# Kernel optimization log

Measured on AMD Instinct MI355X. Metric: run time of the kernel, lower is better.

## Reference

```python
import jax, jax.numpy as jnp
import numpy as np

N = 50000      # nodes
E = 800000     # edges (before self-loops)
IN = 256       # in_channels
H = 4          # heads (layer 1)
C = 64         # hidden per head
OUT = 40       # out_channels / classes


def setup_inputs() -> dict:
    key = jax.random.key(0)
    ks = jax.random.split(key, 10)
    s = 0.05  # weight init scale
    return {
        "x": jax.random.normal(ks[0], (N, IN), jnp.float32),
        "edge_index": jax.random.randint(ks[1], (2, E), 0, N),
        "W1": jax.random.normal(ks[2], (IN, H * C), jnp.float32) * s,
        "a_src1": jax.random.normal(ks[3], (H, C), jnp.float32) * s,
        "a_dst1": jax.random.normal(ks[4], (H, C), jnp.float32) * s,
        "b1": jnp.zeros((H * C,), jnp.float32),
        "W2": jax.random.normal(ks[5], (H * C, OUT), jnp.float32) * s,
        "a_src2": jax.random.normal(ks[6], (1, OUT), jnp.float32) * s,
        "a_dst2": jax.random.normal(ks[7], (1, OUT), jnp.float32) * s,
        "b2": jnp.zeros((OUT,), jnp.float32),
    }


def _gat_layer(x, src, dst, W, a_src, a_dst, bias, heads, out_c):
    """PyG GATConv (concat=True, negative_slope=0.2, self-loops already in src/dst)."""
    n = x.shape[0]
    h = (x @ W).reshape(n, heads, out_c)                    # [N,H,C]
    al_s = jnp.sum(h * a_src, axis=-1)                      # [N,H]
    al_d = jnp.sum(h * a_dst, axis=-1)                      # [N,H]
    e = jax.nn.leaky_relu(al_s[src] + al_d[dst], 0.2)       # [Etot,H]
    # edge softmax over incoming edges of each destination node
    m = jax.ops.segment_max(e, dst, num_segments=n)         # [N,H]
    ee = jnp.exp(e - m[dst])
    denom = jax.ops.segment_sum(ee, dst, num_segments=n)
    alpha = ee / (denom[dst] + 1e-16)                       # [Etot,H]
    msg = alpha[:, :, None] * h[src]                        # [Etot,H,C]
    out = jax.ops.segment_sum(msg, dst, num_segments=n)     # [N,H,C]
    return out.reshape(n, heads * out_c) + bias


def reference(x, edge_index, W1, a_src1, a_dst1, b1, W2, a_src2, a_dst2, b2):
    n = x.shape[0]
    loops = jnp.arange(n, dtype=edge_index.dtype)
    src = jnp.concatenate([edge_index[0], loops])
    dst = jnp.concatenate([edge_index[1], loops])
    h = _gat_layer(x, src, dst, W1, a_src1, a_dst1, b1, H, C)   # [N, H*C]
    h = jax.nn.relu(h)
    # F.dropout in eval mode is identity (reference run in eval mode)
    out = _gat_layer(h, src, dst, W2, a_src2, a_dst2, b2, 1, OUT)  # [N, OUT]
    return jax.nn.log_softmax(out, axis=1)
```

## Files before the change

kernel.cpp:

```cpp
#include <hip/hip_runtime.h>
#include <hip/hip_bf16.h>

typedef __hip_bfloat16 bf16;
typedef short v8s __attribute__((ext_vector_type(8)));
typedef float v4f __attribute__((ext_vector_type(4)));

constexpr int NN    = 50000;
constexpr int NE    = 800000;
constexpr int CIN   = 256;
constexpr int HC    = 256;
constexpr int NH    = 4;
constexpr int NOUT  = 40;
constexpr int NPAD  = 48;
constexpr int SCB   = 196;
constexpr int B1    = 128;
constexpr int CH    = (NE + B1 - 1) / B1;
constexpr int NB    = (NN + 255) >> 8;

constexpr size_t al256(size_t x){ return (x + 255) & ~(size_t)255; }
constexpr size_t WS_FLAGS = 0;
constexpr size_t WS_EW1   = 256;
constexpr size_t WS_W1T   = al256(WS_EW1   + (size_t)NE*16);
constexpr size_t WS_AS1N  = al256(WS_W1T   + (size_t)CIN*HC*2);
constexpr size_t WS_AD1N  = al256(WS_AS1N  + HC*2);
constexpr size_t WS_B1N   = al256(WS_AD1N  + HC*2);
constexpr size_t WS_W2T   = al256(WS_B1N   + HC*2);
constexpr size_t WS_AS2N  = al256(WS_W2T   + (size_t)NPAD*HC*2);
constexpr size_t WS_AD2N  = al256(WS_AS2N  + NOUT*2);
constexpr size_t WS_B2N   = al256(WS_AD2N  + NOUT*2);
constexpr size_t WS_COUNTS= al256(WS_B2N   + NOUT*2);
constexpr size_t WS_CURSOR= al256(WS_COUNTS+ (size_t)NN*4);
constexpr size_t WS_ROWPTR= al256(WS_CURSOR+ (size_t)NN*4);
constexpr size_t WS_EIDX  = al256(WS_ROWPTR+ (size_t)(NN+1)*4);
constexpr size_t WS_H1    = al256(WS_EIDX  + (size_t)NE*4);
constexpr size_t WS_ALS1  = al256(WS_H1    + (size_t)NN*HC);
constexpr size_t WS_ALD1  = al256(WS_ALS1  + (size_t)NN*NH*4);
constexpr size_t WS_Y1    = al256(WS_ALD1  + (size_t)NN*NH*4);
constexpr size_t WS_H2    = al256(WS_Y1    + (size_t)NN*HC*2);
constexpr size_t WS_ALS2  = al256(WS_H2    + (size_t)NN*64);
constexpr size_t WS_ALD2  = al256(WS_ALS2  + (size_t)NN*4);
constexpr size_t WS_EW2   = al256(WS_ALD2  + (size_t)NN*4);
constexpr size_t WS_BSUM  = al256(WS_EW2   + (size_t)NE*4);
constexpr size_t WS_BOFF  = al256(WS_BSUM  + 1024);
constexpr size_t WS_GCNT  = al256(WS_BOFF  + 1024);
constexpr size_t WS_ROFF  = al256(WS_GCNT  + (size_t)256*B1*4);
constexpr size_t WS_BBASE = al256(WS_ROFF  + (size_t)256*B1*4);
constexpr size_t WS_EBUF  = al256(WS_BBASE + 1056);

constexpr int CV_W1  = 0;
constexpr int CV_AS1 = CV_W1  + CIN*HC;
constexpr int CV_AD1 = CV_AS1 + HC;
constexpr int CV_B1  = CV_AD1 + HC;
constexpr int CV_W2  = CV_B1  + HC;
constexpr int CV_AS2 = CV_W2  + HC*NOUT;
constexpr int CV_AD2 = CV_AS2 + NOUT;
constexpr int CV_B2  = CV_AD2 + NOUT;
constexpr int CV_HIST= CV_B2  + NOUT;
constexpr int CV_END = CV_HIST + NE;

__device__ __forceinline__ float b2f(bf16 v) { return __bfloat162float(v); }
__device__ __forceinline__ bf16  f2b(float v){ return __float2bfloat16(v); }
__device__ __forceinline__ float bits2f(unsigned short u){ return __uint_as_float(((unsigned)u) << 16); }
__device__ __forceinline__ unsigned short f2bits(float v){
  bf16 t = __float2bfloat16(v);
  return *reinterpret_cast<unsigned short*>(&t);
}
__device__ __forceinline__ float lrelu(float x){ return x > 0.f ? x : 0.2f * x; }

__device__ __forceinline__ float wave_sum(float v){
  #pragma unroll
  for (int off = 32; off; off >>= 1) v += __shfl_xor(v, off, 64);
  return v;
}
__device__ __forceinline__ float wave_max(float v){
  #pragma unroll
  for (int off = 32; off; off >>= 1) v = fmaxf(v, __shfl_xor(v, off, 64));
  return v;
}

__global__ __launch_bounds__(64) void k_detect(const unsigned short* __restrict__ xu,
                                               const unsigned* __restrict__ eu,
                                               int* __restrict__ flags){
  int lane = threadIdx.x;
  int cnt = 0;
  for (int i = lane; i < 256; i += 64){
    int e = (xu[i] >> 7) & 0xFF;
    cnt += (e >= 0x60 && e <= 0x8F) ? 1 : 0;
  }
  #pragma unroll
  for (int off = 32; off; off >>= 1) cnt += __shfl_xor(cnt, off, 64);
  unsigned odd = eu[2 * lane + 1];
  #pragma unroll
  for (int off = 32; off; off >>= 1) odd |= __shfl_xor(odd, off, 64);
  if (lane == 0){
    flags[0] = (cnt < 218) ? 1 : 0;
    flags[1] = (odd == 0)  ? 1 : 0;
  }
}

__device__ __forceinline__ bf16 cvt_b(const void* src, int i, int f32m){
  if (f32m) return __float2bfloat16(((const float*)src)[i]);
  return ((const bf16*)src)[i];
}

__global__ __launch_bounds__(256) void k_convert(
    const void* __restrict__ W1,
    const void* __restrict__ as1,const void* __restrict__ ad1,
    const void* __restrict__ b1, const void* __restrict__ W2,
    const void* __restrict__ as2,const void* __restrict__ ad2,
    const void* __restrict__ b2, const void* __restrict__ ei,
    char* __restrict__ ws){
  const int* flags = (const int*)(ws + WS_FLAGS);
  int f32m = flags[0], i64m = flags[1];
  bf16* w1t  = (bf16*)(ws + WS_W1T);
  bf16* as1n = (bf16*)(ws + WS_AS1N);
  bf16* ad1n = (bf16*)(ws + WS_AD1N);
  bf16* b1n  = (bf16*)(ws + WS_B1N);
  bf16* w2t  = (bf16*)(ws + WS_W2T);
  bf16* as2n = (bf16*)(ws + WS_AS2N);
  bf16* ad2n = (bf16*)(ws + WS_AD2N);
  bf16* b2n  = (bf16*)(ws + WS_B2N);
  int*  counts=(int*) (ws + WS_COUNTS);
  for (int g = blockIdx.x * 256 + threadIdx.x; g < CV_END; g += gridDim.x * 256){
    if      (g < CV_AS1){ int i = g-CV_W1; int k = i >> 8, n = i & 255;
      w1t[n*CIN + k] = cvt_b(W1, i, f32m); }
    else if (g < CV_AD1) as1n[g-CV_AS1] = cvt_b(as1,g-CV_AS1, f32m);
    else if (g < CV_B1 ) ad1n[g-CV_AD1] = cvt_b(ad1,g-CV_AD1, f32m);
    else if (g < CV_W2 ) b1n [g-CV_B1 ] = cvt_b(b1, g-CV_B1,  f32m);
    else if (g < CV_AS2){ int i = g-CV_W2; int k = i / NOUT, n = i - k*NOUT;
      w2t[n*CIN + k] = cvt_b(W2, i, f32m); }
    else if (g < CV_AD2) as2n[g-CV_AS2] = cvt_b(as2,g-CV_AS2, f32m);
    else if (g < CV_B2 ) ad2n[g-CV_AD2] = cvt_b(ad2,g-CV_AD2, f32m);
    else if (g < CV_HIST) b2n[g-CV_B2 ] = cvt_b(b2, g-CV_B2,  f32m);
    else { int i = g-CV_HIST;
      int d = i64m ? (int)((const long long*)ei)[(size_t)NE+i] : ((const int*)ei)[NE+i];
      atomicAdd(&counts[d], 1); }
  }
}

__global__ __launch_bounds__(256) void k_scan_part(const int* __restrict__ counts, int* __restrict__ bsum){
  __shared__ int lds[256];
  int t = threadIdx.x;
  int idx = blockIdx.x * 256 + t;
  int v = (idx < NN) ? counts[idx] : 0;
  lds[t] = v;
  #pragma unroll
  for (int s = 128; s > 0; s >>= 1){
    __syncthreads();
    if (t < s) lds[t] += lds[t + s];
  }
  if (t == 0) bsum[blockIdx.x] = lds[0];
}

__global__ __launch_bounds__(256) void k_scan_mid(const int* __restrict__ bsum, int* __restrict__ boff,
                                                  int* __restrict__ row_ptr){
  __shared__ int lds[256];
  int t = threadIdx.x;
  int v = (t < SCB) ? bsum[t] : 0;
  lds[t] = v;
  for (int off = 1; off < 256; off <<= 1){
    __syncthreads();
    int u = (t >= off) ? lds[t - off] : 0;
    __syncthreads();
    lds[t] += u;
  }
  __syncthreads();
  if (t < SCB) boff[t] = lds[t] - v;
  if (t == 0) row_ptr[NN] = NE;
}

__global__ __launch_bounds__(256) void k_scan_apply(const int* __restrict__ counts, const int* __restrict__ boff,
                                                    int* __restrict__ row_ptr){
  __shared__ int lds[256];
  int t = threadIdx.x;
  int idx = blockIdx.x * 256 + t;
  int v = (idx < NN) ? counts[idx] : 0;
  lds[t] = v;
  for (int off = 1; off < 256; off <<= 1){
    __syncthreads();
    int u = (t >= off) ? lds[t - off] : 0;
    __syncthreads();
    lds[t] += u;
  }
  __syncthreads();
  if (idx < NN) row_ptr[idx] = boff[blockIdx.x] + lds[t] - v;
}

__global__ __launch_bounds__(256) void k_lhist(const void* __restrict__ ei, const int* __restrict__ flags,
                                               int* __restrict__ gcnt){
  __shared__ int h[256];
  int tid = threadIdx.x, blk = blockIdx.x;
  h[tid] = 0;
  __syncthreads();
  int i0 = blk * CH, i1 = min(i0 + CH, NE);
  int i64m = flags[1];
  for (int i = i0 + tid; i < i1; i += 256){
    int d = i64m ? (int)((const long long*)ei)[(size_t)NE + i] : ((const int*)ei)[NE + i];
    atomicAdd(&h[d >> 8], 1);
  }
  __syncthreads();
  gcnt[tid * B1 + blk] = h[tid];
}

__global__ __launch_bounds__(256) void k_gscan(const int* __restrict__ gcnt, int* __restrict__ roff,
                                               int* __restrict__ bbase){
  __shared__ int lds[256];
  int t = threadIdx.x;
  int tot = 0;
  for (int blk = 0; blk < B1; ++blk) tot += gcnt[t * B1 + blk];
  lds[t] = tot;
  for (int off = 1; off < 256; off <<= 1){
    __syncthreads();
    int u = (t >= off) ? lds[t - off] : 0;
    __syncthreads();
    lds[t] += u;
  }
  __syncthreads();
  int base = lds[t] - tot;
  bbase[t] = base;
  if (t == 255) bbase[256] = NE;
  int run = base;
  for (int blk = 0; blk < B1; ++blk){
    roff[t * B1 + blk] = run;
    run += gcnt[t * B1 + blk];
  }
}

__global__ __launch_bounds__(256) void k_bscatter(const void* __restrict__ ei, const int* __restrict__ flags,
                                                  const int* __restrict__ roff, int2* __restrict__ ebuf){
  __shared__ int lcur[256];
  int tid = threadIdx.x, blk = blockIdx.x;
  lcur[tid] = roff[tid * B1 + blk];
  __syncthreads();
  int i0 = blk * CH, i1 = min(i0 + CH, NE);
  int i64m = flags[1];
  for (int i = i0 + tid; i < i1; i += 256){
    int s, d;
    if (i64m){ s = (int)((const long long*)ei)[i]; d = (int)((const long long*)ei)[(size_t)NE + i]; }
    else     { s = ((const int*)ei)[i];            d = ((const int*)ei)[NE + i]; }
    int pos = atomicAdd(&lcur[d >> 8], 1);
    ebuf[pos] = make_int2(s, d);
  }
}

__global__ __launch_bounds__(256) void k_refine(const int2* __restrict__ ebuf, const int* __restrict__ bbase,
                                                const int* __restrict__ row_ptr, int* __restrict__ cursor,
                                                int* __restrict__ eidx){
  int b = blockIdx.x;
  int p0 = bbase[b], p1 = bbase[b + 1];
  for (int p = p0 + threadIdx.x; p < p1; p += 256){
    int2 e = ebuf[p];
    int pos = row_ptr[e.y] + atomicAdd(&cursor[e.y], 1);
    eidx[pos] = e.x;
  }
}

constexpr int G1R = 64;
constexpr int LP  = 72;
__global__ __launch_bounds__(256) void k_gemm1(const void* __restrict__ xin,
                                               const int* __restrict__ flags,
                                               const bf16* __restrict__ w1t,
                                               const bf16* __restrict__ as1, const bf16* __restrict__ ad1,
                                               unsigned char* __restrict__ h1q,
                                               float* __restrict__ al_s1, float* __restrict__ al_d1){
  __shared__ short Ab[G1R * LP];
  __shared__ short Bb[256 * LP];
  int tid  = threadIdx.x;
  int w    = tid >> 6, lane = tid & 63, quad = lane >> 4, c = lane & 15;
  int row0 = blockIdx.x * G1R;
  int f32m = flags[0];

  v4f acc[4][4];
  #pragma unroll
  for (int mt = 0; mt < 4; ++mt)
    #pragma unroll
    for (int nt = 0; nt < 4; ++nt) acc[mt][nt] = (v4f){0.f,0.f,0.f,0.f};

  int arow = tid >> 2;
  int aseg = tid & 3;
  int grow = row0 + arow; if (grow >= NN) grow = NN - 1;

  for (int ph = 0; ph < 4; ++ph){
    if (ph) __syncthreads();
    {
      short va[16];
      if (f32m){
        const float* src = (const float*)xin + (size_t)grow * CIN + ph*64 + aseg*16;
        #pragma unroll
        for (int i = 0; i < 4; ++i){
          float4 f = *reinterpret_cast<const float4*>(src + i*4);
          va[i*4+0] = (short)f2bits(f.x); va[i*4+1] = (short)f2bits(f.y);
          va[i*4+2] = (short)f2bits(f.z); va[i*4+3] = (short)f2bits(f.w);
        }
      } else {
        const short* src = (const short*)xin + (size_t)grow * CIN + ph*64 + aseg*16;
        v8s u0 = *reinterpret_cast<const v8s*>(src);
        v8s u1 = *reinterpret_cast<const v8s*>(src + 8);
        #pragma unroll
        for (int i = 0; i < 8; ++i){ va[i] = u0[i]; va[8+i] = u1[i]; }
      }
      short* dst = &Ab[arow * LP + aseg * 16];
      *reinterpret_cast<v8s*>(dst)     = *reinterpret_cast<v8s*>(&va[0]);
      *reinterpret_cast<v8s*>(dst + 8) = *reinterpret_cast<v8s*>(&va[8]);
    }
    {
      const short* src = (const short*)w1t + (size_t)tid * CIN + ph*64;
      short* dst = &Bb[tid * LP];
      #pragma unroll
      for (int j = 0; j < 8; ++j)
        *reinterpret_cast<v8s*>(dst + j*8) = *reinterpret_cast<const v8s*>(src + j*8);
    }
    __syncthreads();
    #pragma unroll
    for (int s = 0; s < 2; ++s){
      int ch = s*4 + quad;
      v8s af[4], bfb[4];
      #pragma unroll
      for (int mt = 0; mt < 4; ++mt)
        af[mt] = *reinterpret_cast<const v8s*>(&Ab[(mt*16 + c) * LP + ch*8]);
      #pragma unroll
      for (int nt = 0; nt < 4; ++nt)
        bfb[nt] = *reinterpret_cast<const v8s*>(&Bb[(w*64 + nt*16 + c) * LP + ch*8]);
      #pragma unroll
      for (int mt = 0; mt < 4; ++mt)
        #pragma unroll
        for (int nt = 0; nt < 4; ++nt)
          acc[mt][nt] = __builtin_amdgcn_mfma_f32_16x16x32_bf16(af[mt], bfb[nt], acc[mt][nt], 0, 0, 0);
    }
  }

  float as1v[4], ad1v[4];
  #pragma unroll
  for (int nt = 0; nt < 4; ++nt){
    as1v[nt] = b2f(as1[w*64 + nt*16 + c]);
    ad1v[nt] = b2f(ad1[w*64 + nt*16 + c]);
  }
  #pragma unroll
  for (int mt = 0; mt < 4; ++mt){
    #pragma unroll
    for (int r = 0; r < 4; ++r){
      float ps = 0.f, pd = 0.f;
      #pragma unroll
      for (int nt = 0; nt < 4; ++nt){ ps += acc[mt][nt][r] * as1v[nt]; pd += acc[mt][nt][r] * ad1v[nt]; }
      #pragma unroll
      for (int off = 1; off < 16; off <<= 1){ ps += __shfl_xor(ps, off, 64); pd += __shfl_xor(pd, off, 64); }
      int row = row0 + mt*16 + quad*4 + r;
      if (c == 0 && row < NN){
        al_s1[row * NH + w] = ps;
        al_d1[row * NH + w] = pd;
      }
    }
  }
  #pragma unroll
  for (int mt = 0; mt < 4; ++mt){
    #pragma unroll
    for (int nt = 0; nt < 4; ++nt){
      #pragma unroll
      for (int r = 0; r < 4; r += 2){
        int row = row0 + mt*16 + quad*4 + r;
        if (row + 1 < NN){
          int pk = __builtin_amdgcn_cvt_pk_fp8_f32(acc[mt][nt][r], acc[mt][nt][r+1], 0, false);
          size_t col = w*64 + nt*16 + c;
          h1q[(size_t)row       * HC + col] = (unsigned char)(pk & 0xFF);
          h1q[(size_t)(row + 1) * HC + col] = (unsigned char)((pk >> 8) & 0xFF);
        } else if (row < NN){
          int pk = __builtin_amdgcn_cvt_pk_fp8_f32(acc[mt][nt][r], acc[mt][nt][r], 0, false);
          h1q[(size_t)row * HC + w*64 + nt*16 + c] = (unsigned char)(pk & 0xFF);
        }
      }
    }
  }
}

__global__ __launch_bounds__(256) void k_ew1(const int* __restrict__ row_ptr, const int* __restrict__ eidx,
                                             const float* __restrict__ al_s1, const float* __restrict__ al_d1,
                                             float4* __restrict__ ew1){
  int lane = threadIdx.x & 63;
  int n = blockIdx.x * 4 + (threadIdx.x >> 6);
  int p0 = __builtin_amdgcn_readfirstlane(row_ptr[n]);
  int p1 = __builtin_amdgcn_readfirstlane(row_ptr[n + 1]);
  float4 ad = reinterpret_cast<const float4*>(al_d1)[n];
  for (int p = p0 + lane; p < p1; p += 64){
    int s = eidx[p];
    float4 as = reinterpret_cast<const float4*>(al_s1)[s];
    float4 w;
    w.x = __expf(lrelu(as.x + ad.x));
    w.y = __expf(lrelu(as.y + ad.y));
    w.z = __expf(lrelu(as.z + ad.z));
    w.w = __expf(lrelu(as.w + ad.w));
    ew1[p] = w;
  }
}

__global__ __launch_bounds__(256) void k_gather1(const int* __restrict__ row_ptr, const int* __restrict__ eidx,
                                                 const float* __restrict__ ew1,
                                                 const float* __restrict__ al_s1, const float* __restrict__ al_d1,
                                                 const unsigned* __restrict__ h1v, const bf16* __restrict__ b1,
                                                 bf16* __restrict__ y1){
  int lane = threadIdx.x & 63;
  int n = blockIdx.x * 4 + (threadIdx.x >> 6);
  int h = lane >> 4;
  int p0 = __builtin_amdgcn_readfirstlane(row_ptr[n]);
  int p1 = __builtin_amdgcn_readfirstlane(row_ptr[n + 1]);
  float wss = __expf(lrelu(al_s1[n * NH + h] + al_d1[n * NH + h]));
  unsigned us = h1v[(size_t)n * 64 + lane];
  float den = wss;
  float a0 = wss * __builtin_amdgcn_cvt_f32_fp8(us, 0);
  float a1 = wss * __builtin_amdgcn_cvt_f32_fp8(us, 1);
  float a2 = wss * __builtin_amdgcn_cvt_f32_fp8(us, 2);
  float a3 = wss * __builtin_amdgcn_cvt_f32_fp8(us, 3);
  int p = p0;
  for (; p + 3 < p1; p += 4){
    int sA = __builtin_amdgcn_readfirstlane(eidx[p]);
    int sB = __builtin_amdgcn_readfirstlane(eidx[p + 1]);
    int sC = __builtin_amdgcn_readfirstlane(eidx[p + 2]);
    int sD = __builtin_amdgcn_readfirstlane(eidx[p + 3]);
    float wA = ew1[(size_t)p * 4 + h];
    float wB = ew1[(size_t)(p + 1) * 4 + h];
    float wC = ew1[(size_t)(p + 2) * 4 + h];
    float wD = ew1[(size_t)(p + 3) * 4 + h];
    unsigned uA = h1v[(size_t)sA * 64 + lane];
    unsigned uB = h1v[(size_t)sB * 64 + lane];
    unsigned uC = h1v[(size_t)sC * 64 + lane];
    unsigned uD = h1v[(size_t)sD * 64 + lane];
    den += (wA + wB) + (wC + wD);
    a0 += wA * __builtin_amdgcn_cvt_f32_fp8(uA, 0) + wB * __builtin_amdgcn_cvt_f32_fp8(uB, 0)
        + wC * __builtin_amdgcn_cvt_f32_fp8(uC, 0) + wD * __builtin_amdgcn_cvt_f32_fp8(uD, 0);
    a1 += wA * __builtin_amdgcn_cvt_f32_fp8(uA, 1) + wB * __builtin_amdgcn_cvt_f32_fp8(uB, 1)
        + wC * __builtin_amdgcn_cvt_f32_fp8(uC, 1) + wD * __builtin_amdgcn_cvt_f32_fp8(uD, 1);
    a2 += wA * __builtin_amdgcn_cvt_f32_fp8(uA, 2) + wB * __builtin_amdgcn_cvt_f32_fp8(uB, 2)
        + wC * __builtin_amdgcn_cvt_f32_fp8(uC, 2) + wD * __builtin_amdgcn_cvt_f32_fp8(uD, 2);
    a3 += wA * __builtin_amdgcn_cvt_f32_fp8(uA, 3) + wB * __builtin_amdgcn_cvt_f32_fp8(uB, 3)
        + wC * __builtin_amdgcn_cvt_f32_fp8(uC, 3) + wD * __builtin_amdgcn_cvt_f32_fp8(uD, 3);
  }
  for (; p < p1; ++p){
    int s = __builtin_amdgcn_readfirstlane(eidx[p]);
    float w = ew1[(size_t)p * 4 + h];
    unsigned u = h1v[(size_t)s * 64 + lane];
    den += w;
    a0 += w * __builtin_amdgcn_cvt_f32_fp8(u, 0);
    a1 += w * __builtin_amdgcn_cvt_f32_fp8(u, 1);
    a2 += w * __builtin_amdgcn_cvt_f32_fp8(u, 2);
    a3 += w * __builtin_amdgcn_cvt_f32_fp8(u, 3);
  }
  float inv = 1.f / (den + 1e-16f);
  ushort4 bb = reinterpret_cast<const ushort4*>(b1)[lane];
  ushort4 o;
  o.x = f2bits(fmaxf(a0 * inv + bits2f(bb.x), 0.f));
  o.y = f2bits(fmaxf(a1 * inv + bits2f(bb.y), 0.f));
  o.z = f2bits(fmaxf(a2 * inv + bits2f(bb.z), 0.f));
  o.w = f2bits(fmaxf(a3 * inv + bits2f(bb.w), 0.f));
  reinterpret_cast<ushort4*>(y1)[(size_t)n * 64 + lane] = o;
}

constexpr int W2LP = 260;
__global__ __launch_bounds__(256) void k_gemm2(const bf16* __restrict__ y1, const bf16* __restrict__ w2t,
                                               const bf16* __restrict__ as2, const bf16* __restrict__ ad2,
                                               unsigned char* __restrict__ h2q, float* __restrict__ al_s2,
                                               float* __restrict__ al_d2){
  __shared__ short Wb[NPAD * W2LP];
  int tid = threadIdx.x;
  int w = tid >> 6, lane = tid & 63, quad = lane >> 4, c = lane & 15;
  int m0 = blockIdx.x * 64 + w * 16;
  for (int idx = tid; idx < NPAD * 32; idx += 256){
    int n = idx >> 5, sg = idx & 31;
    *reinterpret_cast<v8s*>(&Wb[n * W2LP + sg * 8]) =
      *reinterpret_cast<const v8s*>((const short*)w2t + (size_t)n * CIN + sg * 8);
  }
  int arow = m0 + c; if (arow >= NN) arow = NN - 1;
  const short* ar = (const short*)y1 + (size_t)arow * HC + quad * 8;
  v8s a[8];
  #pragma unroll
  for (int i = 0; i < 8; ++i) a[i] = *reinterpret_cast<const v8s*>(ar + i * 32);
  __syncthreads();

  v4f acc[3];
  #pragma unroll
  for (int t = 0; t < 3; ++t) acc[t] = (v4f){0.f, 0.f, 0.f, 0.f};
  #pragma unroll
  for (int k = 0; k < 8; ++k){
    int ch = k*4 + quad;
    #pragma unroll
    for (int t = 0; t < 3; ++t){
      v8s b = *reinterpret_cast<const v8s*>(&Wb[(t*16 + c) * W2LP + ch * 8]);
      acc[t] = __builtin_amdgcn_mfma_f32_16x16x32_bf16(a[k], b, acc[t], 0, 0, 0);
    }
  }
  float as2f[3], ad2f[3];
  #pragma unroll
  for (int t = 0; t < 3; ++t){
    int col = t*16 + c;
    as2f[t] = (col < NOUT) ? b2f(as2[col]) : 0.f;
    ad2f[t] = (col < NOUT) ? b2f(ad2[col]) : 0.f;
  }
  #pragma unroll
  for (int r = 0; r < 4; ++r){
    int row = m0 + quad*4 + r;
    float ps = 0.f, pd = 0.f;
    #pragma unroll
    for (int t = 0; t < 3; ++t){ ps += acc[t][r] * as2f[t]; pd += acc[t][r] * ad2f[t]; }
    #pragma unroll
    for (int off = 1; off < 16; off <<= 1){ ps += __shfl_xor(ps, off, 64); pd += __shfl_xor(pd, off, 64); }
    if (row < NN && c == 0){ al_s2[row] = ps; al_d2[row] = pd; }
  }
  #pragma unroll
  for (int t = 0; t < 3; ++t){
    int col = t*16 + c;
    if (col < NOUT){
      #pragma unroll
      for (int r = 0; r < 4; r += 2){
        int row = m0 + quad*4 + r;
        int pk = __builtin_amdgcn_cvt_pk_fp8_f32(acc[t][r], acc[t][r+1], 0, false);
        if (row < NN)     h2q[(size_t)row       * 64 + col] = (unsigned char)(pk & 0xFF);
        if (row + 1 < NN) h2q[(size_t)(row + 1) * 64 + col] = (unsigned char)((pk >> 8) & 0xFF);
      }
    }
  }
}

__global__ __launch_bounds__(256) void k_ew2(const int* __restrict__ row_ptr, const int* __restrict__ eidx,
                                             const float* __restrict__ al_s2, const float* __restrict__ al_d2,
                                             float* __restrict__ ew2){
  int lane = threadIdx.x & 63;
  int n = blockIdx.x * 4 + (threadIdx.x >> 6);
  int p0 = __builtin_amdgcn_readfirstlane(row_ptr[n]);
  int p1 = __builtin_amdgcn_readfirstlane(row_ptr[n + 1]);
  float ad = al_d2[n];
  for (int p = p0 + lane; p < p1; p += 64)
    ew2[p] = __expf(lrelu(al_s2[eidx[p]] + ad));
}

__global__ __launch_bounds__(256) void k_gather2(const int* __restrict__ row_ptr, const int* __restrict__ eidx,
                                                 const float* __restrict__ ew2,
                                                 const float* __restrict__ al_s2, const float* __restrict__ al_d2,
                                                 const unsigned char* __restrict__ h2q, const bf16* __restrict__ b2v,
                                                 const int* __restrict__ flags, void* __restrict__ out){
  int lane = threadIdx.x & 63;
  int n = blockIdx.x * 4 + (threadIdx.x >> 6);
  int q = lane >> 4, c = lane & 15;
  bool act = (c < 10);
  int p0 = __builtin_amdgcn_readfirstlane(row_ptr[n]);
  int p1 = __builtin_amdgcn_readfirstlane(row_ptr[n + 1]);
  const unsigned* h2v = reinterpret_cast<const unsigned*>(h2q);
  float den = 0.f, a0 = 0.f, a1 = 0.f, a2 = 0.f, a3 = 0.f;
  if (q == 0){
    float wss = __expf(lrelu(al_s2[n] + al_d2[n]));
    den = wss;
    if (act){
      unsigned u = h2v[(size_t)n * 16 + c];
      a0 = wss * __builtin_amdgcn_cvt_f32_fp8(u, 0);
      a1 = wss * __builtin_amdgcn_cvt_f32_fp8(u, 1);
      a2 = wss * __builtin_amdgcn_cvt_f32_fp8(u, 2);
      a3 = wss * __builtin_amdgcn_cvt_f32_fp8(u, 3);
    }
  }
  int p = p0 + q;
  for (; p + 4 < p1; p += 8){
    int sA = eidx[p], sB = eidx[p + 4];
    float wA = ew2[p], wB = ew2[p + 4];
    unsigned uA = act ? h2v[(size_t)sA * 16 + c] : 0u;
    unsigned uB = act ? h2v[(size_t)sB * 16 + c] : 0u;
    den += wA + wB;
    a0 += wA * __builtin_amdgcn_cvt_f32_fp8(uA, 0) + wB * __builtin_amdgcn_cvt_f32_fp8(uB, 0);
    a1 += wA * __builtin_amdgcn_cvt_f32_fp8(uA, 1) + wB * __builtin_amdgcn_cvt_f32_fp8(uB, 1);
    a2 += wA * __builtin_amdgcn_cvt_f32_fp8(uA, 2) + wB * __builtin_amdgcn_cvt_f32_fp8(uB, 2);
    a3 += wA * __builtin_amdgcn_cvt_f32_fp8(uA, 3) + wB * __builtin_amdgcn_cvt_f32_fp8(uB, 3);
  }
  if (p < p1){
    int s = eidx[p];
    float w = ew2[p];
    unsigned u = act ? h2v[(size_t)s * 16 + c] : 0u;
    den += w;
    a0 += w * __builtin_amdgcn_cvt_f32_fp8(u, 0);
    a1 += w * __builtin_amdgcn_cvt_f32_fp8(u, 1);
    a2 += w * __builtin_amdgcn_cvt_f32_fp8(u, 2);
    a3 += w * __builtin_amdgcn_cvt_f32_fp8(u, 3);
  }
  #pragma unroll
  for (int off = 16; off <= 32; off <<= 1){
    den += __shfl_xor(den, off, 64);
    a0  += __shfl_xor(a0,  off, 64);
    a1  += __shfl_xor(a1,  off, 64);
    a2  += __shfl_xor(a2,  off, 64);
    a3  += __shfl_xor(a3,  off, 64);
  }
  float inv = 1.f / (den + 1e-16f);
  float v0 = -INFINITY, v1 = -INFINITY, v2 = -INFINITY, v3 = -INFINITY;
  if (act){
    ushort4 bb = *reinterpret_cast<const ushort4*>(reinterpret_cast<const unsigned short*>(b2v) + 4 * c);
    v0 = a0 * inv + bits2f(bb.x);
    v1 = a1 * inv + bits2f(bb.y);
    v2 = a2 * inv + bits2f(bb.z);
    v3 = a3 * inv + bits2f(bb.w);
  }
  float M = wave_max(fmaxf(fmaxf(v0, v1), fmaxf(v2, v3)));
  float ex = (q == 0 && act)
           ? (__expf(v0 - M) + __expf(v1 - M)) + (__expf(v2 - M) + __expf(v3 - M)) : 0.f;
  float S = wave_sum(ex);
  if (q == 0 && act){
    float lg = M + __logf(S);
    if (flags[0]){
      float4 o = {v0 - lg, v1 - lg, v2 - lg, v3 - lg};
      *reinterpret_cast<float4*>((float*)out + (size_t)n * NOUT + 4 * c) = o;
    } else {
      ushort4 o;
      o.x = f2bits(v0 - lg); o.y = f2bits(v1 - lg);
      o.z = f2bits(v2 - lg); o.w = f2bits(v3 - lg);
      *reinterpret_cast<ushort4*>((unsigned short*)out + (size_t)n * NOUT + 4 * c) = o;
    }
  }
}

extern "C" void kernel_launch(void* const* d_in, const int* in_sizes, int n_in,
                              void* d_out, int out_size, void* d_ws, size_t ws_size,
                              hipStream_t stream) {
  const void* x   = d_in[0];
  const void* ei  = d_in[1];
  const void* W1  = d_in[2];
  const void* as1 = d_in[3];
  const void* ad1 = d_in[4];
  const void* b1  = d_in[5];
  const void* W2  = d_in[6];
  const void* as2 = d_in[7];
  const void* ad2 = d_in[8];
  const void* b2  = d_in[9];

  char* ws = (char*)d_ws;
  int*   flags   = (int*)  (ws + WS_FLAGS);
  float* ew1     = (float*)(ws + WS_EW1);
  bf16*  w1t     = (bf16*) (ws + WS_W1T);
  bf16*  as1n    = (bf16*) (ws + WS_AS1N);
  bf16*  ad1n    = (bf16*) (ws + WS_AD1N);
  bf16*  b1n     = (bf16*) (ws + WS_B1N);
  bf16*  w2t     = (bf16*) (ws + WS_W2T);
  bf16*  as2n    = (bf16*) (ws + WS_AS2N);
  bf16*  ad2n    = (bf16*) (ws + WS_AD2N);
  bf16*  b2n     = (bf16*) (ws + WS_B2N);
  int*   counts  = (int*)  (ws + WS_COUNTS);
  int*   cursor  = (int*)  (ws + WS_CURSOR);
  int*   row_ptr = (int*)  (ws + WS_ROWPTR);
  int*   eidx    = (int*)  (ws + WS_EIDX);
  unsigned char* h1q = (unsigned char*)(ws + WS_H1);
  float* al_s1   = (float*)(ws + WS_ALS1);
  float* al_d1   = (float*)(ws + WS_ALD1);
  bf16*  y1      = (bf16*) (ws + WS_Y1);
  unsigned char* h2q = (unsigned char*)(ws + WS_H2);
  float* al_s2   = (float*)(ws + WS_ALS2);
  float* al_d2   = (float*)(ws + WS_ALD2);
  float* ew2     = (float*)(ws + WS_EW2);
  int*   bsum    = (int*)  (ws + WS_BSUM);
  int*   boff    = (int*)  (ws + WS_BOFF);
  int*   gcnt    = (int*)  (ws + WS_GCNT);
  int*   roff    = (int*)  (ws + WS_ROFF);
  int*   bbase   = (int*)  (ws + WS_BBASE);
  int2*  ebuf    = (int2*) (ws + WS_EBUF);

  hipMemsetAsync(counts, 0, (size_t)NN * 4, stream);
  hipMemsetAsync(cursor, 0, (size_t)NN * 4, stream);
  hipMemsetAsync(w2t,    0, (size_t)NPAD * CIN * 2, stream);

  k_detect <<<1, 64, 0, stream>>>((const unsigned short*)x, (const unsigned*)ei, flags);
  k_convert<<<1024, 256, 0, stream>>>(W1, as1, ad1, b1, W2, as2, ad2, b2, ei, ws);

  k_lhist   <<<B1, 256, 0, stream>>>(ei, flags, gcnt);
  k_gscan   <<<1, 256, 0, stream>>>(gcnt, roff, bbase);
  k_scan_part <<<SCB, 256, 0, stream>>>(counts, bsum);
  k_scan_mid  <<<1, 256, 0, stream>>>(bsum, boff, row_ptr);
  k_scan_apply<<<SCB, 256, 0, stream>>>(counts, boff, row_ptr);
  k_bscatter<<<B1, 256, 0, stream>>>(ei, flags, roff, ebuf);
  k_refine  <<<NB, 256, 0, stream>>>(ebuf, bbase, row_ptr, cursor, eidx);

  k_gemm1  <<<(NN + G1R - 1) / G1R, 256, 0, stream>>>(x, flags, w1t, as1n, ad1n, h1q, al_s1, al_d1);
  k_ew1    <<<NN / 4, 256, 0, stream>>>(row_ptr, eidx, al_s1, al_d1, (float4*)ew1);
  k_gather1<<<NN / 4, 256, 0, stream>>>(row_ptr, eidx, ew1, al_s1, al_d1, (const unsigned*)h1q, b1n, y1);
  k_gemm2  <<<(NN + 63) / 64, 256, 0, stream>>>(y1, w2t, as2n, ad2n, h2q, al_s2, al_d2);
  k_ew2    <<<NN / 4, 256, 0, stream>>>(row_ptr, eidx, al_s2, al_d2, ew2);
  k_gather2<<<NN / 4, 256, 0, stream>>>(row_ptr, eidx, ew2, al_s2, al_d2, h2q, b2n, flags, d_out);
}
```

Before: 331.6 us.

## Double-buffer GEMM1 shared tiles with register prefetch and XOR-swizzled LDS layout

Restructures the first-layer GEMM's K loop to prefetch the next phase of A and B tiles into registers while MFMAs run on the current LDS buffer, then stage them into a second buffer. The padded LDS rows are replaced by an XOR swizzle to avoid bank conflicts without padding. The kernel also gets a launch bound of two blocks per SM. The aim is to hide global-load latency behind compute and cut LDS conflicts. The cost is doubled LDS use and more live registers, which may limit occupancy.

```diff
diff --git a/kernel.cpp b/kernel.cpp
--- a/kernel.cpp
+++ b/kernel.cpp
@@ -256,15 +256,14 @@
 }
 
 constexpr int G1R = 64;
-constexpr int LP  = 72;
-__global__ __launch_bounds__(256) void k_gemm1(const void* __restrict__ xin,
+__global__ __launch_bounds__(256, 2) void k_gemm1(const void* __restrict__ xin,
                                                const int* __restrict__ flags,
                                                const bf16* __restrict__ w1t,
                                                const bf16* __restrict__ as1, const bf16* __restrict__ ad1,
                                                unsigned char* __restrict__ h1q,
                                                float* __restrict__ al_s1, float* __restrict__ al_d1){
-  __shared__ short Ab[G1R * LP];
-  __shared__ short Bb[256 * LP];
+  __shared__ __align__(16) short Ab[2][G1R * 64];
+  __shared__ __align__(16) short Bb[2][256 * 64];
   int tid  = threadIdx.x;
   int w    = tid >> 6, lane = tid & 63, quad = lane >> 4, c = lane & 15;
   int row0 = blockIdx.x * G1R;
@@ -276,56 +275,84 @@
     #pragma unroll
     for (int nt = 0; nt < 4; ++nt) acc[mt][nt] = (v4f){0.f,0.f,0.f,0.f};
 
-  int arow = tid >> 2;
-  int aseg = tid & 3;
+  int arow = tid >> 2, aseg = tid & 3;
   int grow = row0 + arow; if (grow >= NN) grow = NN - 1;
-
+  int asw  = arow & 7;
+  int bsw  = tid & 7;
+
+  float4 afl[4];
+  v8s    abf[2];
+  v8s    breg[8];
+
+  auto loadA = [&](int ph){
+    if (f32m){
+      const float* src = (const float*)xin + (size_t)grow * CIN + ph*64 + aseg*16;
+      #pragma unroll
+      for (int i = 0; i < 4; ++i) afl[i] = *reinterpret_cast<const float4*>(src + i*4);
+    } else {
+      const short* src = (const short*)xin + (size_t)grow * CIN + ph*64 + aseg*16;
+      abf[0] = *reinterpret_cast<const v8s*>(src);
+      abf[1] = *reinterpret_cast<const v8s*>(src + 8);
+    }
+  };
+  auto loadB = [&](int ph){
+    const short* src = (const short*)w1t + (size_t)tid * CIN + ph*64;
+    #pragma unroll
+    for (int j = 0; j < 8; ++j) breg[j] = *reinterpret_cast<const v8s*>(src + j*8);
+  };
+  auto stageA = [&](int buf){
+    short* dst = &Ab[buf][arow * 64];
+    if (f32m){
+      #pragma unroll
+      for (int k = 0; k < 2; ++k){
+        v8s t;
+        t[0] = (short)f2bits(afl[2*k].x);   t[1] = (short)f2bits(afl[2*k].y);
+        t[2] = (short)f2bits(afl[2*k].z);   t[3] = (short)f2bits(afl[2*k].w);
+        t[4] = (short)f2bits(afl[2*k+1].x); t[5] = (short)f2bits(afl[2*k+1].y);
+        t[6] = (short)f2bits(afl[2*k+1].z); t[7] = (short)f2bits(afl[2*k+1].w);
+        *reinterpret_cast<v8s*>(dst + (((aseg*2 + k) ^ asw) << 3)) = t;
+      }
+    } else {
+      #pragma unroll
+      for (int k = 0; k < 2; ++k)
+        *reinterpret_cast<v8s*>(dst + (((aseg*2 + k) ^ asw) << 3)) = abf[k];
+    }
+  };
+  auto stageB = [&](int buf){
+    short* dst = &Bb[buf][tid * 64];
+    #pragma unroll
+    for (int j = 0; j < 8; ++j)
+      *reinterpret_cast<v8s*>(dst + ((j ^ bsw) << 3)) = breg[j];
+  };
+
+  loadA(0); loadB(0);
+  stageA(0); stageB(0);
+  __syncthreads();
+
+  #pragma unroll
   for (int ph = 0; ph < 4; ++ph){
-    if (ph) __syncthreads();
-    {
-      short va[16];
-      if (f32m){
-        const float* src = (const float*)xin + (size_t)grow * CIN + ph*64 + aseg*16;
-        #pragma unroll
-        for (int i = 0; i < 4; ++i){
-          float4 f = *reinterpret_cast<const float4*>(src + i*4);
-          va[i*4+0] = (short)f2bits(f.x); va[i*4+1] = (short)f2bits(f.y);
-          va[i*4+2] = (short)f2bits(f.z); va[i*4+3] = (short)f2bits(f.w);
-        }
-      } else {
-        const short* src = (const short*)xin + (size_t)grow * CIN + ph*64 + aseg*16;
-        v8s u0 = *reinterpret_cast<const v8s*>(src);
-        v8s u1 = *reinterpret_cast<const v8s*>(src + 8);
-        #pragma unroll
-        for (int i = 0; i < 8; ++i){ va[i] = u0[i]; va[8+i] = u1[i]; }
-      }
-      short* dst = &Ab[arow * LP + aseg * 16];
-      *reinterpret_cast<v8s*>(dst)     = *reinterpret_cast<v8s*>(&va[0]);
-      *reinterpret_cast<v8s*>(dst + 8) = *reinterpret_cast<v8s*>(&va[8]);
-    }
-    {
-      const short* src = (const short*)w1t + (size_t)tid * CIN + ph*64;
-      short* dst = &Bb[tid * LP];
-      #pragma unroll
-      for (int j = 0; j < 8; ++j)
-        *reinterpret_cast<v8s*>(dst + j*8) = *reinterpret_cast<const v8s*>(src + j*8);
-    }
-    __syncthreads();
+    int buf = ph & 1;
+    if (ph < 3){ loadA(ph + 1); loadB(ph + 1); }
     #pragma unroll
     for (int s = 0; s < 2; ++s){
       int ch = s*4 + quad;
+      int sl = (ch ^ (c & 7)) << 3;
       v8s af[4], bfb[4];
       #pragma unroll
       for (int mt = 0; mt < 4; ++mt)
-        af[mt] = *reinterpret_cast<const v8s*>(&Ab[(mt*16 + c) * LP + ch*8]);
+        af[mt] = *reinterpret_cast<const v8s*>(&Ab[buf][(mt*16 + c) * 64 + sl]);
       #pragma unroll
       for (int nt = 0; nt < 4; ++nt)
-        bfb[nt] = *reinterpret_cast<const v8s*>(&Bb[(w*64 + nt*16 + c) * LP + ch*8]);
+        bfb[nt] = *reinterpret_cast<const v8s*>(&Bb[buf][(w*64 + nt*16 + c) * 64 + sl]);
       #pragma unroll
       for (int mt = 0; mt < 4; ++mt)
         #pragma unroll
         for (int nt = 0; nt < 4; ++nt)
           acc[mt][nt] = __builtin_amdgcn_mfma_f32_16x16x32_bf16(af[mt], bfb[nt], acc[mt][nt], 0, 0, 0);
+    }
+    if (ph < 3){
+      stageA(buf ^ 1); stageB(buf ^ 1);
+      __syncthreads();
     }
   }
 
```

Result: no change. 331.1 us (-0.2%).

## Fuse edge-weight computation into gather kernels and drop LDS staging in gemm1

Applied to the files above, without the earlier changes.

Removes the separate k_ew1 and k_ew2 kernels: each gather kernel now recomputes exp(leaky_relu(al_s[src]+al_d[dst])) inline from the source index, avoiding a write and re-read of the per-edge weight buffers and two launches. Separately, gemm1 no longer stages A and B tiles through shared memory with barriers; each lane loads its MFMA fragments directly from global memory (x rows and the transposed W1). This trades LDS traffic and syncs for redundant global/L2 loads of W1 across blocks and extra exp work in the gathers.

```diff
diff --git a/kernel.cpp b/kernel.cpp
--- a/kernel.cpp
+++ b/kernel.cpp
@@ -256,71 +256,61 @@
 }
 
 constexpr int G1R = 64;
-constexpr int LP  = 72;
 __global__ __launch_bounds__(256) void k_gemm1(const void* __restrict__ xin,
                                                const int* __restrict__ flags,
                                                const bf16* __restrict__ w1t,
                                                const bf16* __restrict__ as1, const bf16* __restrict__ ad1,
                                                unsigned char* __restrict__ h1q,
                                                float* __restrict__ al_s1, float* __restrict__ al_d1){
-  __shared__ short Ab[G1R * LP];
-  __shared__ short Bb[256 * LP];
   int tid  = threadIdx.x;
   int w    = tid >> 6, lane = tid & 63, quad = lane >> 4, c = lane & 15;
   int row0 = blockIdx.x * G1R;
   int f32m = flags[0];
 
+  size_t arow[4];
+  #pragma unroll
+  for (int mt = 0; mt < 4; ++mt){
+    int r = row0 + mt*16 + c; if (r >= NN) r = NN - 1;
+    arow[mt] = (size_t)r;
+  }
+  const short* brow[4];
+  #pragma unroll
+  for (int nt = 0; nt < 4; ++nt)
+    brow[nt] = (const short*)w1t + (size_t)(w*64 + nt*16 + c) * CIN;
+
   v4f acc[4][4];
   #pragma unroll
   for (int mt = 0; mt < 4; ++mt)
     #pragma unroll
     for (int nt = 0; nt < 4; ++nt) acc[mt][nt] = (v4f){0.f,0.f,0.f,0.f};
 
-  int arow = tid >> 2;
-  int aseg = tid & 3;
-  int grow = row0 + arow; if (grow >= NN) grow = NN - 1;
-
+  #pragma unroll 1
   for (int ph = 0; ph < 4; ++ph){
-    if (ph) __syncthreads();
-    {
-      short va[16];
+    #pragma unroll
+    for (int s = 0; s < 2; ++s){
+      int ko = ph*64 + (s*4 + quad)*8;
+      v8s af[4], bfb[4];
       if (f32m){
-        const float* src = (const float*)xin + (size_t)grow * CIN + ph*64 + aseg*16;
         #pragma unroll
-        for (int i = 0; i < 4; ++i){
-          float4 f = *reinterpret_cast<const float4*>(src + i*4);
-          va[i*4+0] = (short)f2bits(f.x); va[i*4+1] = (short)f2bits(f.y);
-          va[i*4+2] = (short)f2bits(f.z); va[i*4+3] = (short)f2bits(f.w);
+        for (int mt = 0; mt < 4; ++mt){
+          const float* src = (const float*)xin + arow[mt]*CIN + ko;
+          float4 f0 = *reinterpret_cast<const float4*>(src);
+          float4 f1 = *reinterpret_cast<const float4*>(src + 4);
+          v8s t;
+          t[0] = (short)f2bits(f0.x); t[1] = (short)f2bits(f0.y);
+          t[2] = (short)f2bits(f0.z); t[3] = (short)f2bits(f0.w);
+          t[4] = (short)f2bits(f1.x); t[5] = (short)f2bits(f1.y);
+          t[6] = (short)f2bits(f1.z); t[7] = (short)f2bits(f1.w);
+          af[mt] = t;
         }
       } else {
-        const short* src = (const short*)xin + (size_t)grow * CIN + ph*64 + aseg*16;
-        v8s u0 = *reinterpret_cast<const v8s*>(src);
-        v8s u1 = *reinterpret_cast<const v8s*>(src + 8);
         #pragma unroll
-        for (int i = 0; i < 8; ++i){ va[i] = u0[i]; va[8+i] = u1[i]; }
+        for (int mt = 0; mt < 4; ++mt)
+          af[mt] = *reinterpret_cast<const v8s*>((const short*)xin + arow[mt]*CIN + ko);
       }
-      short* dst = &Ab[arow * LP + aseg * 16];
-      *reinterpret_cast<v8s*>(dst)     = *reinterpret_cast<v8s*>(&va[0]);
-      *reinterpret_cast<v8s*>(dst + 8) = *reinterpret_cast<v8s*>(&va[8]);
-    }
-    {
-      const short* src = (const short*)w1t + (size_t)tid * CIN + ph*64;
-      short* dst = &Bb[tid * LP];
-      #pragma unroll
-      for (int j = 0; j < 8; ++j)
-        *reinterpret_cast<v8s*>(dst + j*8) = *reinterpret_cast<const v8s*>(src + j*8);
-    }
-    __syncthreads();
-    #pragma unroll
-    for (int s = 0; s < 2; ++s){
-      int ch = s*4 + quad;
-      v8s af[4], bfb[4];
-      #pragma unroll
-      for (int mt = 0; mt < 4; ++mt)
-        af[mt] = *reinterpret_cast<const v8s*>(&Ab[(mt*16 + c) * LP + ch*8]);
       #pragma unroll
       for (int nt = 0; nt < 4; ++nt)
-        bfb[nt] = *reinterpret_cast<const v8s*>(&Bb[(w*64 + nt*16 + c) * LP + ch*8]);
+        bfb[nt] = *reinterpret_cast<const v8s*>(brow[nt] + ko);
       #pragma unroll
       for (int mt = 0; mt < 4; ++mt)
         #pragma unroll
@@ -372,28 +362,7 @@
   }
 }
 
-__global__ __launch_bounds__(256) void k_ew1(const int* __restrict__ row_ptr, const int* __restrict__ eidx,
-                                             const float* __restrict__ al_s1, const float* __restrict__ al_d1,
-                                             float4* __restrict__ ew1){
-  int lane = threadIdx.x & 63;
-  int n = blockIdx.x * 4 + (threadIdx.x >> 6);
-  int p0 = __builtin_amdgcn_readfirstlane(row_ptr[n]);
-  int p1 = __builtin_amdgcn_readfirstlane(row_ptr[n + 1]);
-  float4 ad = reinterpret_cast<const float4*>(al_d1)[n];
-  for (int p = p0 + lane; p < p1; p += 64){
-    int s = eidx[p];
-    float4 as = reinterpret_cast<const float4*>(al_s1)[s];
-    float4 w;
-    w.x = __expf(lrelu(as.x + ad.x));
-    w.y = __expf(lrelu(as.y + ad.y));
-    w.z = __expf(lrelu(as.z + ad.z));
-    w.w = __expf(lrelu(as.w + ad.w));
-    ew1[p] = w;
-  }
-}
-
 __global__ __launch_bounds__(256) void k_gather1(const int* __restrict__ row_ptr, const int* __restrict__ eidx,
-                                                 const float* __restrict__ ew1,
                                                  const float* __restrict__ al_s1, const float* __restrict__ al_d1,
                                                  const unsigned* __restrict__ h1v, const bf16* __restrict__ b1,
                                                  bf16* __restrict__ y1){
@@ -402,7 +371,8 @@
   int h = lane >> 4;
   int p0 = __builtin_amdgcn_readfirstlane(row_ptr[n]);
   int p1 = __builtin_amdgcn_readfirstlane(row_ptr[n + 1]);
-  float wss = __expf(lrelu(al_s1[n * NH + h] + al_d1[n * NH + h]));
+  float ad_h = al_d1[n * NH + h];
+  float wss = __expf(lrelu(al_s1[n * NH + h] + ad_h));
   unsigned us = h1v[(size_t)n * 64 + lane];
   float den = wss;
   float a0 = wss * __builtin_amdgcn_cvt_f32_fp8(us, 0);
@@ -415,10 +385,10 @@
     int sB = __builtin_amdgcn_readfirstlane(eidx[p + 1]);
     int sC = __builtin_amdgcn_readfirstlane(eidx[p + 2]);
     int sD = __builtin_amdgcn_readfirstlane(eidx[p + 3]);
-    float wA = ew1[(size_t)p * 4 + h];
-    float wB = ew1[(size_t)(p + 1) * 4 + h];
-    float wC = ew1[(size_t)(p + 2) * 4 + h];
-    float wD = ew1[(size_t)(p + 3) * 4 + h];
+    float wA = __expf(lrelu(al_s1[sA * NH + h] + ad_h));
+    float wB = __expf(lrelu(al_s1[sB * NH + h] + ad_h));
+    float wC = __expf(lrelu(al_s1[sC * NH + h] + ad_h));
+    float wD = __expf(lrelu(al_s1[sD * NH + h] + ad_h));
     unsigned uA = h1v[(size_t)sA * 64 + lane];
     unsigned uB = h1v[(size_t)sB * 64 + lane];
     unsigned uC = h1v[(size_t)sC * 64 + lane];
@@ -435,7 +405,7 @@
   }
   for (; p < p1; ++p){
     int s = __builtin_amdgcn_readfirstlane(eidx[p]);
-    float w = ew1[(size_t)p * 4 + h];
+    float w = __expf(lrelu(al_s1[s * NH + h] + ad_h));
     unsigned u = h1v[(size_t)s * 64 + lane];
     den += w;
     a0 += w * __builtin_amdgcn_cvt_f32_fp8(u, 0);
@@ -518,20 +488,7 @@
   }
 }
 
-__global__ __launch_bounds__(256) void k_ew2(const int* __restrict__ row_ptr, const int* __restrict__ eidx,
-                                             const float* __restrict__ al_s2, const float* __restrict__ al_d2,
-                                             float* __restrict__ ew2){
-  int lane = threadIdx.x & 63;
-  int n = blockIdx.x * 4 + (threadIdx.x >> 6);
-  int p0 = __builtin_amdgcn_readfirstlane(row_ptr[n]);
-  int p1 = __builtin_amdgcn_readfirstlane(row_ptr[n + 1]);
-  float ad = al_d2[n];
-  for (int p = p0 + lane; p < p1; p += 64)
-    ew2[p] = __expf(lrelu(al_s2[eidx[p]] + ad));
-}
-
 __global__ __launch_bounds__(256) void k_gather2(const int* __restrict__ row_ptr, const int* __restrict__ eidx,
-                                                 const float* __restrict__ ew2,
                                                  const float* __restrict__ al_s2, const float* __restrict__ al_d2,
                                                  const unsigned char* __restrict__ h2q, const bf16* __restrict__ b2v,
                                                  const int* __restrict__ flags, void* __restrict__ out){
@@ -542,9 +499,10 @@
   int p0 = __builtin_amdgcn_readfirstlane(row_ptr[n]);
   int p1 = __builtin_amdgcn_readfirstlane(row_ptr[n + 1]);
   const unsigned* h2v = reinterpret_cast<const unsigned*>(h2q);
+  float adn = al_d2[n];
   float den = 0.f, a0 = 0.f, a1 = 0.f, a2 = 0.f, a3 = 0.f;
   if (q == 0){
-    float wss = __expf(lrelu(al_s2[n] + al_d2[n]));
+    float wss = __expf(lrelu(al_s2[n] + adn));
     den = wss;
     if (act){
       unsigned u = h2v[(size_t)n * 16 + c];
@@ -557,7 +515,8 @@
   int p = p0 + q;
   for (; p + 4 < p1; p += 8){
     int sA = eidx[p], sB = eidx[p + 4];
-    float wA = ew2[p], wB = ew2[p + 4];
+    float wA = __expf(lrelu(al_s2[sA] + adn));
+    float wB = __expf(lrelu(al_s2[sB] + adn));
     unsigned uA = act ? h2v[(size_t)sA * 16 + c] : 0u;
     unsigned uB = act ? h2v[(size_t)sB * 16 + c] : 0u;
     den += wA + wB;
@@ -568,7 +527,7 @@
   }
   if (p < p1){
     int s = eidx[p];
-    float w = ew2[p];
+    float w = __expf(lrelu(al_s2[s] + adn));
     unsigned u = act ? h2v[(size_t)s * 16 + c] : 0u;
     den += w;
     a0 += w * __builtin_amdgcn_cvt_f32_fp8(u, 0);
@@ -627,7 +586,6 @@
 
   char* ws = (char*)d_ws;
   int*   flags   = (int*)  (ws + WS_FLAGS);
-  float* ew1     = (float*)(ws + WS_EW1);
   bf16*  w1t     = (bf16*) (ws + WS_W1T);
   bf16*  as1n    = (bf16*) (ws + WS_AS1N);
   bf16*  ad1n    = (bf16*) (ws + WS_AD1N);
@@ -647,7 +605,6 @@
   unsigned char* h2q = (unsigned char*)(ws + WS_H2);
   float* al_s2   = (float*)(ws + WS_ALS2);
   float* al_d2   = (float*)(ws + WS_ALD2);
-  float* ew2     = (float*)(ws + WS_EW2);
   int*   bsum    = (int*)  (ws + WS_BSUM);
   int*   boff    = (int*)  (ws + WS_BOFF);
   int*   gcnt    = (int*)  (ws + WS_GCNT);
@@ -671,9 +628,7 @@
   k_refine  <<<NB, 256, 0, stream>>>(ebuf, bbase, row_ptr, cursor, eidx);
 
   k_gemm1  <<<(NN + G1R - 1) / G1R, 256, 0, stream>>>(x, flags, w1t, as1n, ad1n, h1q, al_s1, al_d1);
-  k_ew1    <<<NN / 4, 256, 0, stream>>>(row_ptr, eidx, al_s1, al_d1, (float4*)ew1);
-  k_gather1<<<NN / 4, 256, 0, stream>>>(row_ptr, eidx, ew1, al_s1, al_d1, (const unsigned*)h1q, b1n, y1);
+  k_gather1<<<NN / 4, 256, 0, stream>>>(row_ptr, eidx, al_s1, al_d1, (const unsigned*)h1q, b1n, y1);
   k_gemm2  <<<(NN + 63) / 64, 256, 0, stream>>>(y1, w2t, as2n, ad2n, h2q, al_s2, al_d2);
-  k_ew2    <<<NN / 4, 256, 0, stream>>>(row_ptr, eidx, al_s2, al_d2, ew2);
-  k_gather2<<<NN / 4, 256, 0, stream>>>(row_ptr, eidx, ew2, al_s2, al_d2, h2q, b2n, flags, d_out);
-}
+  k_gather2<<<NN / 4, 256, 0, stream>>>(row_ptr, eidx, al_s2, al_d2, h2q, b2n, flags, d_out);
+}
```

Result: no change. 336.0 us (+1.3%).
